# Kernel tuning notes

Hardware: AMD Instinct MI355X
Metric: run time of the kernel (lower is better)

Reference implementation:

```python
import jax, jax.numpy as jnp
import numpy as np

B, S, D, H, TOPK = 8, 128, 1024, 4096, 256


def _linear_params(key, out_d, in_d):
    # torch nn.Linear default init: U(-1/sqrt(fan_in), 1/sqrt(fan_in))
    bound = 1.0 / np.sqrt(in_d)
    kw, kb = jax.random.split(key)
    w = jax.random.uniform(kw, (out_d, in_d), minval=-bound, maxval=bound, dtype=jnp.float32)
    b = jax.random.uniform(kb, (out_d,), minval=-bound, maxval=bound, dtype=jnp.float32)
    return w, b


def setup_inputs() -> dict:
    key = jax.random.key(0)
    ks = jax.random.split(key, 6)
    inputs = jax.random.normal(ks[0], (B, S, D), dtype=jnp.float32)
    up_prev_w, up_prev_b = _linear_params(ks[1], H, D)   # self.up[0]
    up_curr_w, up_curr_b = _linear_params(ks[2], H, D)   # self.up[1]
    gate_w1, gate_b1 = _linear_params(ks[3], H, D)       # gates[0][0]
    gate_w2, gate_b2 = _linear_params(ks[4], H, H)       # gates[0][2]
    down_w, down_b = _linear_params(ks[5], D, H)         # self.down[1]
    return {
        'inputs': inputs,
        'up_prev_w': up_prev_w, 'up_prev_b': up_prev_b,
        'up_curr_w': up_curr_w, 'up_curr_b': up_curr_b,
        'gate_w1': gate_w1, 'gate_b1': gate_b1,
        'gate_w2': gate_w2, 'gate_b2': gate_b2,
        'down_w': down_w, 'down_b': down_b,
        'current_depth': 1,
    }


def reference(inputs, up_prev_w, up_prev_b, up_curr_w, up_curr_b,
              gate_w1, gate_b1, gate_w2, gate_b2, down_w, down_b,
              current_depth):
    x = inputs  # [B, S, D]
    # Gate MLP: Linear(D,H) -> ReLU -> Linear(H,H)  => scores [B, S, H]
    g = jax.nn.relu(jnp.einsum('bsd,hd->bsh', x, gate_w1) + gate_b1)
    scores = jnp.einsum('bsh,gh->bsg', g, gate_w2) + gate_b2
    # topk over flattened [S*H] scores per batch element
    k = min(TOPK * S, S * H)
    _, flat_idx = jax.lax.top_k(scores.reshape(B, S * H), k)  # [B, k]
    hidden_idx = flat_idx % H  # row indices into the weight matrices
    # Selected rows get prev layer's weights/bias (duplicate indices write the
    # same value, so a boolean-mask select is exactly equivalent to the scatter).
    sel = jnp.zeros((B, H), dtype=bool).at[jnp.arange(B)[:, None], hidden_idx].set(True)
    mod_w = jnp.where(sel[:, :, None], up_prev_w[None], up_curr_w[None])  # [B, H, D]
    mod_b = jnp.where(sel, up_prev_b[None], up_curr_b[None])              # [B, H]
    # Per-sample matmul: inputs @ mod_w^T + bias
    h = jnp.einsum('bsd,bhd->bsh', x, mod_w) + mod_b[:, None, :]
    h = jax.nn.gelu(h, approximate=False)  # torch GELU (exact)
    # dropout p=0 (eval) -> identity
    return jnp.einsum('bsh,dh->bsd', h, down_w) + down_b
```

## Files before the change

### kernel.cpp

```cpp
#include <hip/hip_runtime.h>
#include <hip/hip_bf16.h>

#define B_  8
#define S_  128
#define D_  1024
#define H_  4096
#define M_  (B_ * S_)
#define NSCORE   (M_ * H_)
#define PERBATCH (S_ * H_)
#define TOPK_K   (256 * S_)
#define BAND_CAP 8192
#define MARGIN   4e-4f

#define AS1 __attribute__((address_space(1)))
#define AS3 __attribute__((address_space(3)))

#define G_OFF    0u
#define SC_OFF   16777216u
#define GHI_OFF  33554432u
#define GLO_OFF  41943040u
#define XHI_OFF  50331648u
#define XLO_OFF  52428800u
#define W1H_OFF  54525952u
#define W1L_OFF  62914560u
#define W2H_OFF  54525952u
#define W2L_OFF  88080384u
#define WPB_OFF  54525952u
#define WCB_OFF  62914560u
#define WDB_OFF  71303168u
#define ACT_OFF  79691776u
#define H8_OFF   121634816u
#define H16_OFF  121700352u
#define SEL_OFF  123797504u
#define CNT_OFF  123928576u
#define PART_OFF 123929088u
#define BIDX_OFF 123933184u
#define BVAL_OFF 124195328u

typedef __attribute__((ext_vector_type(8))) short short8;
typedef __attribute__((ext_vector_type(4))) float f32x4;

__device__ __forceinline__ unsigned tokey(float f) {
    unsigned u = __float_as_uint(f);
    return (u & 0x80000000u) ? ~u : (u | 0x80000000u);
}
__device__ __forceinline__ float keytofloat(unsigned k) {
    unsigned u = (k & 0x80000000u) ? (k & 0x7FFFFFFFu) : ~k;
    return __uint_as_float(u);
}
__device__ __forceinline__ unsigned short bfbits(float f) {
    __hip_bfloat16 h = __float2bfloat16(f);
    return *(unsigned short*)&h;
}

__global__ __launch_bounds__(256) void split_kernel(const float* __restrict__ in,
                                                    unsigned short* __restrict__ hi,
                                                    unsigned short* __restrict__ lo, int n4) {
    int i = blockIdx.x * 256 + threadIdx.x;
    if (i >= n4) return;
    float4 v = *(const float4*)(in + (size_t)i * 4);
    unsigned short h0 = bfbits(v.x), h1 = bfbits(v.y), h2 = bfbits(v.z), h3 = bfbits(v.w);
    ushort4 hv = {h0, h1, h2, h3};
    float r0 = v.x - __bfloat162float(*(__hip_bfloat16*)&h0);
    float r1 = v.y - __bfloat162float(*(__hip_bfloat16*)&h1);
    float r2 = v.z - __bfloat162float(*(__hip_bfloat16*)&h2);
    float r3 = v.w - __bfloat162float(*(__hip_bfloat16*)&h3);
    ushort4 lv = {bfbits(r0), bfbits(r1), bfbits(r2), bfbits(r3)};
    *(ushort4*)(hi + (size_t)i*4) = hv;
    *(ushort4*)(lo + (size_t)i*4) = lv;
}

__global__ __launch_bounds__(256) void f2bf3_kernel(const float* __restrict__ s0,
                                                    const float* __restrict__ s1,
                                                    const float* __restrict__ s2,
                                                    unsigned short* __restrict__ d0,
                                                    unsigned short* __restrict__ d1,
                                                    unsigned short* __restrict__ d2) {
    const int Q = H_ * D_ / 4;
    int i = blockIdx.x * 256 + threadIdx.x;
    int w = i / Q, j = i - w * Q;
    const float* s = (w == 0) ? s0 : (w == 1) ? s1 : s2;
    unsigned short* d = (w == 0) ? d0 : (w == 1) ? d1 : d2;
    float4 v = *(const float4*)(s + (size_t)j * 4);
    ushort4 o = {bfbits(v.x), bfbits(v.y), bfbits(v.z), bfbits(v.w)};
    *(ushort4*)(d + (size_t)j * 4) = o;
}

template <int EPI>
__global__ __launch_bounds__(256) void gemm_split_kernel(const short* __restrict__ Ahg,
                                                         const short* __restrict__ Alg,
                                                         const short* __restrict__ Bhg,
                                                         const short* __restrict__ Blg,
                                                         const float* __restrict__ bias,
                                                         int K,
                                                         float* __restrict__ C,
                                                         unsigned short* __restrict__ hi,
                                                         unsigned short* __restrict__ lo) {
    __shared__ short lAh[64*64], lAl[64*64], lBh[128*64], lBl[128*64];
    const int tid = threadIdx.x, lane = tid & 63, wave = tid >> 6;
    const int row0 = blockIdx.y * 64, col0 = blockIdx.x * 128;
    f32x4 acc[4][2] = {};
    for (int kt = 0; kt < K; kt += 64) {
        #pragma unroll
        for (int q = 0; q < 2; q++) {
            int l = q * 256 + tid;
            int r = l >> 3, cg = ((l & 7) ^ (r & 7)) * 8;
            size_t go = (size_t)(row0 + r) * K + kt + cg;
            __builtin_amdgcn_global_load_lds((const AS1 unsigned*)(Ahg + go),
                (AS3 unsigned*)(lAh + l * 8), 16, 0, 0);
            __builtin_amdgcn_global_load_lds((const AS1 unsigned*)(Alg + go),
                (AS3 unsigned*)(lAl + l * 8), 16, 0, 0);
        }
        #pragma unroll
        for (int q = 0; q < 4; q++) {
            int l = q * 256 + tid;
            int r = l >> 3, cg = ((l & 7) ^ (r & 7)) * 8;
            size_t go = (size_t)(col0 + r) * K + kt + cg;
            __builtin_amdgcn_global_load_lds((const AS1 unsigned*)(Bhg + go),
                (AS3 unsigned*)(lBh + l * 8), 16, 0, 0);
            __builtin_amdgcn_global_load_lds((const AS1 unsigned*)(Blg + go),
                (AS3 unsigned*)(lBl + l * 8), 16, 0, 0);
        }
        __syncthreads();
        #pragma unroll
        for (int kk = 0; kk < 2; kk++) {
            const int cb = kk * 4 + (lane >> 4);
            short8 ah[4], al[4], bh[2], bl[2];
            #pragma unroll
            for (int i = 0; i < 4; i++) {
                int r = i * 16 + (lane & 15);
                int s = (r * 8 + (cb ^ (r & 7))) * 8;
                ah[i] = *(const short8*)(lAh + s);
                al[i] = *(const short8*)(lAl + s);
            }
            #pragma unroll
            for (int j = 0; j < 2; j++) {
                int r = wave * 32 + j * 16 + (lane & 15);
                int s = (r * 8 + (cb ^ (r & 7))) * 8;
                bh[j] = *(const short8*)(lBh + s);
                bl[j] = *(const short8*)(lBl + s);
            }
            #pragma unroll
            for (int i = 0; i < 4; i++)
                #pragma unroll
                for (int j = 0; j < 2; j++) {
                    acc[i][j] = __builtin_amdgcn_mfma_f32_16x16x32_bf16(al[i], bh[j], acc[i][j], 0, 0, 0);
                    acc[i][j] = __builtin_amdgcn_mfma_f32_16x16x32_bf16(ah[i], bl[j], acc[i][j], 0, 0, 0);
                    acc[i][j] = __builtin_amdgcn_mfma_f32_16x16x32_bf16(ah[i], bh[j], acc[i][j], 0, 0, 0);
                }
        }
        __syncthreads();
    }
    #pragma unroll
    for (int i = 0; i < 4; i++) {
        int row = row0 + i * 16 + (lane >> 4) * 4;
        #pragma unroll
        for (int j = 0; j < 2; j++) {
            int col = col0 + wave * 32 + j * 16 + (lane & 15);
            float bv = bias[col];
            #pragma unroll
            for (int r = 0; r < 4; r++) {
                float v = acc[i][j][r] + bv;
                size_t o = (size_t)(row + r) * H_ + col;
                if (EPI == 1) {
                    v = fmaxf(v, 0.0f);
                    C[o] = v;
                    unsigned short hb = bfbits(v);
                    hi[o] = hb;
                    lo[o] = bfbits(v - __bfloat162float(*(__hip_bfloat16*)&hb));
                } else {
                    C[o] = v;
                }
            }
        }
    }
}

__global__ __launch_bounds__(256) void bgemm_bt_kernel(const short* __restrict__ A,
                                                       const short* __restrict__ B0,
                                                       const short* __restrict__ B1,
                                                       float* __restrict__ C0,
                                                       float* __restrict__ C1,
                                                       int N, int K) {
    const short* Bw = (blockIdx.z == 0) ? B0 : B1;
    float*       C  = (blockIdx.z == 0) ? C0 : C1;
    __shared__ short As[128 * 32];
    __shared__ short Bs[128 * 32];
    const int tid = threadIdx.x, lane = tid & 63, wave = tid >> 6;
    const int wr = wave >> 1, wc = wave & 1;
    const int row0 = blockIdx.y * 128, col0 = blockIdx.x * 128;
    const int r_ld = tid >> 2, c_ld = (tid & 3) * 8;
    f32x4 acc[4][4] = {};
    for (int kt = 0; kt < K; kt += 32) {
        #pragma unroll
        for (int half = 0; half < 2; half++) {
            int r = half * 64 + r_ld;
            __builtin_amdgcn_global_load_lds(
                (const AS1 unsigned*)(A + (size_t)(row0 + r) * K + kt + c_ld),
                (AS3 unsigned*)(As + r * 32 + c_ld), 16, 0, 0);
            __builtin_amdgcn_global_load_lds(
                (const AS1 unsigned*)(Bw + (size_t)(col0 + r) * K + kt + c_ld),
                (AS3 unsigned*)(Bs + r * 32 + c_ld), 16, 0, 0);
        }
        __syncthreads();
        short8 af[4], bfr[4];
        #pragma unroll
        for (int t = 0; t < 4; t++) {
            af[t]  = *(const short8*)(As + (wr*64 + t*16 + (lane & 15)) * 32 + (lane >> 4) * 8);
            bfr[t] = *(const short8*)(Bs + (wc*64 + t*16 + (lane & 15)) * 32 + (lane >> 4) * 8);
        }
        #pragma unroll
        for (int tm = 0; tm < 4; tm++)
            #pragma unroll
            for (int tn = 0; tn < 4; tn++)
                acc[tm][tn] = __builtin_amdgcn_mfma_f32_16x16x32_bf16(af[tm], bfr[tn], acc[tm][tn], 0, 0, 0);
        __syncthreads();
    }
    #pragma unroll
    for (int tm = 0; tm < 4; tm++) {
        int row = row0 + wr*64 + tm*16 + (lane >> 4) * 4;
        #pragma unroll
        for (int tn = 0; tn < 4; tn++) {
            int col = col0 + wc*64 + tn*16 + (lane & 15);
            #pragma unroll
            for (int r = 0; r < 4; r++)
                C[(size_t)(row + r) * N + col] = acc[tm][tn][r];
        }
    }
}

__global__ __launch_bounds__(256) void bgemm_down_kernel(const short* __restrict__ A,
                                                         const short* __restrict__ Bw,
                                                         float* __restrict__ P) {
    __shared__ short As[128 * 32];
    __shared__ short Bs[128 * 32];
    const int tid = threadIdx.x, lane = tid & 63, wave = tid >> 6;
    const int wr = wave >> 1, wc = wave & 1;
    const int row0 = blockIdx.y * 128, col0 = blockIdx.x * 128;
    const int k0 = blockIdx.z * (H_ / 4);
    float* C = P + (size_t)blockIdx.z * (M_ * D_);
    const int r_ld = tid >> 2, c_ld = (tid & 3) * 8;
    f32x4 acc[4][4] = {};
    for (int kt = k0; kt < k0 + H_ / 4; kt += 32) {
        #pragma unroll
        for (int half = 0; half < 2; half++) {
            int r = half * 64 + r_ld;
            __builtin_amdgcn_global_load_lds(
                (const AS1 unsigned*)(A + (size_t)(row0 + r) * H_ + kt + c_ld),
                (AS3 unsigned*)(As + r * 32 + c_ld), 16, 0, 0);
            __builtin_amdgcn_global_load_lds(
                (const AS1 unsigned*)(Bw + (size_t)(col0 + r) * H_ + kt + c_ld),
                (AS3 unsigned*)(Bs + r * 32 + c_ld), 16, 0, 0);
        }
        __syncthreads();
        short8 af[4], bfr[4];
        #pragma unroll
        for (int t = 0; t < 4; t++) {
            af[t]  = *(const short8*)(As + (wr*64 + t*16 + (lane & 15)) * 32 + (lane >> 4) * 8);
            bfr[t] = *(const short8*)(Bs + (wc*64 + t*16 + (lane & 15)) * 32 + (lane >> 4) * 8);
        }
        #pragma unroll
        for (int tm = 0; tm < 4; tm++)
            #pragma unroll
            for (int tn = 0; tn < 4; tn++)
                acc[tm][tn] = __builtin_amdgcn_mfma_f32_16x16x32_bf16(af[tm], bfr[tn], acc[tm][tn], 0, 0, 0);
        __syncthreads();
    }
    #pragma unroll
    for (int tm = 0; tm < 4; tm++) {
        int row = row0 + wr*64 + tm*16 + (lane >> 4) * 4;
        #pragma unroll
        for (int tn = 0; tn < 4; tn++) {
            int col = col0 + wc*64 + tn*16 + (lane & 15);
            #pragma unroll
            for (int r = 0; r < 4; r++)
                C[(size_t)(row + r) * D_ + col] = acc[tm][tn][r];
        }
    }
}

__global__ __launch_bounds__(256) void down_merge_kernel(const float* __restrict__ P,
                                                         const float* __restrict__ db,
                                                         float* __restrict__ out) {
    int i = blockIdx.x * 256 + threadIdx.x;
    if (i >= M_ * D_ / 4) return;
    int col = (i * 4) & (D_ - 1);
    float4 a = *(const float4*)(P + (size_t)i * 4);
    float4 b = *(const float4*)(P + (size_t)(M_*D_) + (size_t)i * 4);
    float4 c = *(const float4*)(P + (size_t)(2*M_*D_) + (size_t)i * 4);
    float4 d = *(const float4*)(P + (size_t)(3*M_*D_) + (size_t)i * 4);
    float4 o;
    o.x = a.x + b.x + c.x + d.x + db[col+0];
    o.y = a.y + b.y + c.y + d.y + db[col+1];
    o.z = a.z + b.z + c.z + d.z + db[col+2];
    o.w = a.w + b.w + c.w + d.w + db[col+3];
    *(float4*)(out + (size_t)i * 4) = o;
}

__global__ __launch_bounds__(256) void hist8_kernel(const float* __restrict__ scores,
                                                    unsigned* __restrict__ h8) {
    __shared__ unsigned lh[256];
    const int b = blockIdx.y;
    lh[threadIdx.x] = 0;
    __syncthreads();
    const float* base = scores + ((size_t)b << 19) + (size_t)blockIdx.x * 8192;
    for (int j = threadIdx.x; j < 8192; j += 256) {
        unsigned key = tokey(base[j]);
        atomicAdd(&lh[key >> 24], 1u);
    }
    __syncthreads();
    unsigned v = lh[threadIdx.x];
    if (v) atomicAdd(&h8[(b << 8) + threadIdx.x], v);
}

__global__ __launch_bounds__(256) void scan8_kernel(const unsigned* __restrict__ h8,
                                                    unsigned* __restrict__ prefix1,
                                                    unsigned* __restrict__ above1) {
    int b = blockIdx.x, tid = threadIdx.x;
    __shared__ unsigned S[256];
    __shared__ int tstar;
    S[tid] = h8[(b << 8) + tid];
    __syncthreads();
    for (int off = 1; off < 256; off <<= 1) {
        unsigned a = S[tid];
        unsigned v = (tid + off < 256) ? S[tid + off] : 0u;
        __syncthreads();
        S[tid] = a + v;
        __syncthreads();
    }
    unsigned St = S[tid];
    unsigned Sn = (tid < 255) ? S[tid + 1] : 0u;
    if (St >= TOPK_K && (tid == 255 || Sn < TOPK_K)) tstar = tid;
    __syncthreads();
    if (tid == 0) {
        prefix1[b] = (unsigned)tstar;
        above1[b]  = (tstar < 255) ? S[tstar + 1] : 0u;
    }
}

__global__ __launch_bounds__(256) void hist16_kernel(const float* __restrict__ scores,
                                                     const unsigned* __restrict__ prefix1,
                                                     unsigned* __restrict__ h16) {
    int i = blockIdx.x * 256 + threadIdx.x;
    if (i >= NSCORE) return;
    int b = i >> 19;
    unsigned key = tokey(scores[i]);
    if ((key >> 24) == prefix1[b])
        atomicAdd(&h16[((size_t)b << 16) + ((key >> 8) & 0xFFFFu)], 1u);
}

__global__ __launch_bounds__(256) void scan16_kernel(const unsigned* __restrict__ h16,
                                                     const unsigned* __restrict__ prefix1,
                                                     const unsigned* __restrict__ above1,
                                                     float* __restrict__ Thi,
                                                     float* __restrict__ Tlo) {
    int b = blockIdx.x, tid = threadIdx.x;
    const unsigned* h = h16 + ((size_t)b << 16);
    unsigned k = TOPK_K - above1[b];
    __shared__ unsigned S[256];
    __shared__ int tstar;
    unsigned s = 0;
    const unsigned* seg = h + tid * 256;
    for (int i = 0; i < 256; i++) s += seg[i];
    S[tid] = s;
    __syncthreads();
    for (int off = 1; off < 256; off <<= 1) {
        unsigned a = S[tid];
        unsigned v = (tid + off < 256) ? S[tid + off] : 0u;
        __syncthreads();
        S[tid] = a + v;
        __syncthreads();
    }
    unsigned St = S[tid];
    unsigned Sn = (tid < 255) ? S[tid + 1] : 0u;
    if (St >= k && (tid == 255 || Sn < k)) tstar = tid;
    __syncthreads();
    if (tid == 0) {
        int t = tstar;
        unsigned runn = (t < 255) ? S[t + 1] : 0u;
        unsigned c = (unsigned)t * 256u;
        for (int i = 255; i >= 0; i--) {
            unsigned cc = h[t * 256 + i];
            if (runn + cc >= k) { c = (unsigned)(t * 256 + i); break; }
            runn += cc;
        }
        unsigned P24 = (prefix1[b] << 16) | c;
        float tlo = (P24 < 0x8000u) ? -INFINITY : keytofloat(P24 << 8);
        float thi = (P24 == 0x00FFFFFFu) ? INFINITY
                  : ((P24 + 1u) < 0x8000u ? -INFINITY : keytofloat((P24 + 1u) << 8));
        Thi[b] = thi + MARGIN;
        Tlo[b] = tlo - MARGIN;
    }
}

__global__ __launch_bounds__(256) void classify_kernel(const float* __restrict__ scores,
                                                       const float* __restrict__ Thi,
                                                       const float* __restrict__ Tlo,
                                                       unsigned* __restrict__ sel,
                                                       unsigned* __restrict__ partialCnt,
                                                       unsigned* __restrict__ bandN,
                                                       unsigned* __restrict__ bandIdx) {
    const int b  = blockIdx.z;
    const int h0 = blockIdx.x * 256;
    const int s0 = blockIdx.y * 16;
    const int c  = threadIdx.x;
    const float thi = Thi[b], tlo = Tlo[b];
    unsigned selbit = 0, cnt = 0;
    const float* base = scores + ((size_t)(b * S_ + s0)) * H_ + h0;
    #pragma unroll 4
    for (int j = 0; j < 16; j++) {
        float sv = base[(size_t)j * H_ + c];
        if (sv > thi) { selbit = 1u; cnt++; }
        else if (sv >= tlo) {
            unsigned slot = atomicAdd(&bandN[b], 1u);
            if (slot < BAND_CAP)
                bandIdx[(b << 13) + slot] = (unsigned)(((s0 + j) << 12) | (h0 + c));
        }
    }
    if (selbit) sel[(b << 12) + h0 + c] = 1u;
    __shared__ unsigned red[256];
    red[c] = cnt;
    __syncthreads();
    for (int off = 128; off; off >>= 1) {
        if (c < off) red[c] += red[c + off];
        __syncthreads();
    }
    if (c == 0) partialCnt[b * 128 + blockIdx.y * 16 + blockIdx.x] = red[0];
}

__global__ void finalize_cnt_kernel(const unsigned* __restrict__ partial,
                                    unsigned* __restrict__ certN) {
    int b = threadIdx.x;
    if (b >= B_) return;
    unsigned s = 0;
    for (int i = 0; i < 128; i++) s += partial[b * 128 + i];
    certN[b] = s;
}

__global__ __launch_bounds__(256) void band_exact_kernel(const float* __restrict__ g,
                                                         const float* __restrict__ w2,
                                                         const float* __restrict__ b2,
                                                         const unsigned* __restrict__ bandN,
                                                         const unsigned* __restrict__ bandIdx,
                                                         float* __restrict__ bandVal) {
    int wid = (blockIdx.x * 256 + threadIdx.x) >> 6;
    int lane = threadIdx.x & 63;
    for (int b = 0; b < B_; b++) {
        int n = bandN[b]; if (n > BAND_CAP) n = BAND_CAP;
        for (int j = wid; j < n; j += 1024) {
            unsigned f = bandIdx[(b << 13) + j];
            int m = b * S_ + (int)(f >> 12);
            int h = (int)(f & (H_ - 1));
            const float* gr = g  + (size_t)m * H_;
            const float* wr = w2 + (size_t)h * H_;
            float s = 0.0f;
            for (int cc = lane * 4; cc < H_; cc += 256) {
                float4 a = *(const float4*)(gr + cc);
                float4 w = *(const float4*)(wr + cc);
                s += a.x*w.x + a.y*w.y + a.z*w.z + a.w*w.w;
            }
            #pragma unroll
            for (int off = 32; off; off >>= 1) s += __shfl_xor(s, off);
            if (lane == 0) bandVal[(b << 13) + j] = s + b2[h];
        }
    }
}

__global__ __launch_bounds__(256) void band_select_kernel(const float* __restrict__ bandVal,
                                                          const unsigned* __restrict__ bandIdx,
                                                          const unsigned* __restrict__ bandN,
                                                          const unsigned* __restrict__ certainN,
                                                          unsigned* __restrict__ sel) {
    __shared__ float  sv[BAND_CAP];
    __shared__ unsigned si[BAND_CAP];
    int b = blockIdx.x, tid = threadIdx.x;
    int n = bandN[b]; if (n > BAND_CAP) n = BAND_CAP;
    int r = TOPK_K - (int)certainN[b];
    if (r <= 0) return;
    if (r >= n) {
        for (int j = tid; j < n; j += 256)
            sel[(b << 12) + (bandIdx[(b << 13) + j] & (H_ - 1))] = 1u;
        return;
    }
    for (int j = tid; j < n; j += 256) {
        sv[j] = bandVal[(b << 13) + j];
        si[j] = bandIdx[(b << 13) + j];
    }
    __syncthreads();
    for (int j = tid; j < n; j += 256) {
        float vj = sv[j]; unsigned fj = si[j];
        int rank = 0;
        for (int l = 0; l < n; l++) {
            float vl = sv[l]; unsigned fl = si[l];
            rank += (vl > vj) || (vl == vj && fl < fj);
        }
        if (rank < r) sel[(b << 12) + (fj & (H_ - 1))] = 1u;
    }
}

__global__ __launch_bounds__(256) void act_kernel(const float* __restrict__ hprev,
                                                  const float* __restrict__ hcurr,
                                                  const float* __restrict__ bprev,
                                                  const float* __restrict__ bcurr,
                                                  const unsigned* __restrict__ sel,
                                                  __hip_bfloat16* __restrict__ act) {
    int i = blockIdx.x * 256 + threadIdx.x;
    if (i >= NSCORE) return;
    int h = i & (H_ - 1);
    int b = i >> 19;
    float v = sel[(b << 12) + h] ? (hprev[i] + bprev[h]) : (hcurr[i] + bcurr[h]);
    float gl = 0.5f * v * (1.0f + erff(v * 0.70710678118654752440f));
    act[i] = __float2bfloat16(gl);
}

extern "C" void kernel_launch(void* const* d_in, const int* in_sizes, int n_in,
                              void* d_out, int out_size, void* d_ws, size_t ws_size,
                              hipStream_t stream) {
    const float* x     = (const float*)d_in[0];
    const float* wprev = (const float*)d_in[1];
    const float* bprev = (const float*)d_in[2];
    const float* wcurr = (const float*)d_in[3];
    const float* bcurr = (const float*)d_in[4];
    const float* gw1   = (const float*)d_in[5];
    const float* gb1   = (const float*)d_in[6];
    const float* gw2   = (const float*)d_in[7];
    const float* gb2   = (const float*)d_in[8];
    const float* dw    = (const float*)d_in[9];
    const float* db    = (const float*)d_in[10];
    float* out = (float*)d_out;
    char* ws = (char*)d_ws;

    float* g      = (float*)(ws + G_OFF);
    float* scores = (float*)(ws + SC_OFF);
    float* hprev  = (float*)(ws + G_OFF);
    float* hcurr  = (float*)(ws + SC_OFF);
    float* dpart  = (float*)(ws + GHI_OFF);
    unsigned short* ghi = (unsigned short*)(ws + GHI_OFF);
    unsigned short* glo = (unsigned short*)(ws + GLO_OFF);
    unsigned short* xhi = (unsigned short*)(ws + XHI_OFF);
    unsigned short* xlo = (unsigned short*)(ws + XLO_OFF);
    unsigned short* w1h = (unsigned short*)(ws + W1H_OFF);
    unsigned short* w1l = (unsigned short*)(ws + W1L_OFF);
    unsigned short* w2h = (unsigned short*)(ws + W2H_OFF);
    unsigned short* w2l = (unsigned short*)(ws + W2L_OFF);
    unsigned short* wpb = (unsigned short*)(ws + WPB_OFF);
    unsigned short* wcb = (unsigned short*)(ws + WCB_OFF);
    unsigned short* wdb = (unsigned short*)(ws + WDB_OFF);
    __hip_bfloat16* act = (__hip_bfloat16*)(ws + ACT_OFF);
    unsigned* h8      = (unsigned*)(ws + H8_OFF);
    unsigned* h16     = (unsigned*)(ws + H16_OFF);
    unsigned* sel     = (unsigned*)(ws + SEL_OFF);
    unsigned* certN   = (unsigned*)(ws + CNT_OFF);
    unsigned* bandN   = (unsigned*)(ws + CNT_OFF + 32);
    unsigned* prefix1 = (unsigned*)(ws + CNT_OFF + 64);
    unsigned* above1  = (unsigned*)(ws + CNT_OFF + 96);
    float*    Thi     = (float*)(ws + CNT_OFF + 128);
    float*    Tlo     = (float*)(ws + CNT_OFF + 160);
    unsigned* partCnt = (unsigned*)(ws + PART_OFF);
    unsigned* bandIdx = (unsigned*)(ws + BIDX_OFF);
    float*    bandVal = (float*)(ws + BVAL_OFF);

    hipMemsetAsync(ws + H8_OFF, 0, 65536 + 2097152, stream);
    hipMemsetAsync(ws + SEL_OFF, 0, 131072 + 512 + 4096, stream);

    split_kernel<<<(M_*D_/4 + 255)/256, 256, 0, stream>>>(x,   xhi, xlo, M_*D_/4);
    split_kernel<<<(H_*D_/4 + 255)/256, 256, 0, stream>>>(gw1, w1h, w1l, H_*D_/4);
    gemm_split_kernel<1><<<dim3(H_/128, M_/64), 256, 0, stream>>>(
        (const short*)xhi, (const short*)xlo, (const short*)w1h, (const short*)w1l,
        gb1, D_, g, ghi, glo);
    split_kernel<<<(H_*H_/4 + 255)/256, 256, 0, stream>>>(gw2, w2h, w2l, H_*H_/4);
    gemm_split_kernel<0><<<dim3(H_/128, M_/64), 256, 0, stream>>>(
        (const short*)ghi, (const short*)glo, (const short*)w2h, (const short*)w2l,
        gb2, H_, scores, nullptr, nullptr);

    f2bf3_kernel<<<3*(H_*D_/4)/256, 256, 0, stream>>>(wprev, wcurr, dw, wpb, wcb, wdb);

    hist8_kernel<<<dim3(64, 8), 256, 0, stream>>>(scores, h8);
    scan8_kernel<<<B_, 256, 0, stream>>>(h8, prefix1, above1);
    hist16_kernel<<<NSCORE/256, 256, 0, stream>>>(scores, prefix1, h16);
    scan16_kernel<<<B_, 256, 0, stream>>>(h16, prefix1, above1, Thi, Tlo);

    classify_kernel<<<dim3(16, 8, 8), 256, 0, stream>>>(scores, Thi, Tlo, sel, partCnt, bandN, bandIdx);
    finalize_cnt_kernel<<<1, 64, 0, stream>>>(partCnt, certN);
    band_exact_kernel<<<256, 256, 0, stream>>>(g, gw2, gb2, bandN, bandIdx, bandVal);
    band_select_kernel<<<B_, 256, 0, stream>>>(bandVal, bandIdx, bandN, certN, sel);

    bgemm_bt_kernel<<<dim3(H_/128, M_/128, 2), 256, 0, stream>>>(
        (const short*)xhi, (const short*)wpb, (const short*)wcb, hprev, hcurr, H_, D_);
    act_kernel<<<NSCORE/256, 256, 0, stream>>>(hprev, hcurr, bprev, bcurr, sel, act);
    bgemm_down_kernel<<<dim3(D_/128, M_/128, 4), 256, 0, stream>>>(
        (const short*)act, (const short*)wdb, dpart);
    down_merge_kernel<<<(M_*D_/4 + 255)/256, 256, 0, stream>>>(dpart, db, out);
}
```

Before: 545.2 us.

## Drop split-bf16 for gate GEMM2, fuse histogram, select-gather up GEMM with GELU

```diff
diff --git a/kernel.cpp b/kernel.cpp
--- a/kernel.cpp
+++ b/kernel.cpp
@@ -10,7 +10,7 @@
 #define PERBATCH (S_ * H_)
 #define TOPK_K   (256 * S_)
 #define BAND_CAP 8192
-#define MARGIN   4e-4f
+#define MARGIN   6e-3f
 
 #define AS1 __attribute__((address_space(1)))
 #define AS3 __attribute__((address_space(3)))
@@ -23,8 +23,7 @@
 #define XLO_OFF  52428800u
 #define W1H_OFF  54525952u
 #define W1L_OFF  62914560u
-#define W2H_OFF  54525952u
-#define W2L_OFF  88080384u
+#define W2B_OFF  54525952u
 #define WPB_OFF  54525952u
 #define WCB_OFF  62914560u
 #define WDB_OFF  71303168u
@@ -70,6 +69,15 @@
     *(ushort4*)(lo + (size_t)i*4) = lv;
 }
 
+__global__ __launch_bounds__(256) void f2bf_kernel(const float* __restrict__ in,
+                                                   unsigned short* __restrict__ out, int n4) {
+    int i = blockIdx.x * 256 + threadIdx.x;
+    if (i >= n4) return;
+    float4 v = *(const float4*)(in + (size_t)i * 4);
+    ushort4 o = {bfbits(v.x), bfbits(v.y), bfbits(v.z), bfbits(v.w)};
+    *(ushort4*)(out + (size_t)i * 4) = o;
+}
+
 __global__ __launch_bounds__(256) void f2bf3_kernel(const float* __restrict__ s0,
                                                     const float* __restrict__ s1,
                                                     const float* __restrict__ s2,
@@ -86,26 +94,23 @@
     *(ushort4*)(d + (size_t)j * 4) = o;
 }
 
-template <int EPI>
-__global__ __launch_bounds__(256) void gemm_split_kernel(const short* __restrict__ Ahg,
-                                                         const short* __restrict__ Alg,
-                                                         const short* __restrict__ Bhg,
-                                                         const short* __restrict__ Blg,
-                                                         const float* __restrict__ bias,
-                                                         int K,
-                                                         float* __restrict__ C,
-                                                         unsigned short* __restrict__ hi,
-                                                         unsigned short* __restrict__ lo) {
+__global__ __launch_bounds__(256) void gemm1_kernel(const short* __restrict__ Ahg,
+                                                    const short* __restrict__ Alg,
+                                                    const short* __restrict__ Bhg,
+                                                    const short* __restrict__ Blg,
+                                                    const float* __restrict__ bias,
+                                                    float* __restrict__ C,
+                                                    unsigned short* __restrict__ hi) {
     __shared__ short lAh[64*64], lAl[64*64], lBh[128*64], lBl[128*64];
     const int tid = threadIdx.x, lane = tid & 63, wave = tid >> 6;
     const int row0 = blockIdx.y * 64, col0 = blockIdx.x * 128;
     f32x4 acc[4][2] = {};
-    for (int kt = 0; kt < K; kt += 64) {
+    for (int kt = 0; kt < D_; kt += 64) {
         #pragma unroll
         for (int q = 0; q < 2; q++) {
             int l = q * 256 + tid;
             int r = l >> 3, cg = ((l & 7) ^ (r & 7)) * 8;
-            size_t go = (size_t)(row0 + r) * K + kt + cg;
+            size_t go = (size_t)(row0 + r) * D_ + kt + cg;
             __builtin_amdgcn_global_load_lds((const AS1 unsigned*)(Ahg + go),
                 (AS3 unsigned*)(lAh + l * 8), 16, 0, 0);
             __builtin_amdgcn_global_load_lds((const AS1 unsigned*)(Alg + go),
@@ -115,7 +120,7 @@
         for (int q = 0; q < 4; q++) {
             int l = q * 256 + tid;
             int r = l >> 3, cg = ((l & 7) ^ (r & 7)) * 8;
-            size_t go = (size_t)(col0 + r) * K + kt + cg;
+            size_t go = (size_t)(col0 + r) * D_ + kt + cg;
             __builtin_amdgcn_global_load_lds((const AS1 unsigned*)(Bhg + go),
                 (AS3 unsigned*)(lBh + l * 8), 16, 0, 0);
             __builtin_amdgcn_global_load_lds((const AS1 unsigned*)(Blg + go),
@@ -160,54 +165,123 @@
             float bv = bias[col];
             #pragma unroll
             for (int r = 0; r < 4; r++) {
+                float v = fmaxf(acc[i][j][r] + bv, 0.0f);
+                size_t o = (size_t)(row + r) * H_ + col;
+                C[o] = v;
+                hi[o] = bfbits(v);
+            }
+        }
+    }
+}
+
+__global__ __launch_bounds__(256) void gemm2_kernel(const short* __restrict__ Ahg,
+                                                    const short* __restrict__ Bhg,
+                                                    const float* __restrict__ bias,
+                                                    float* __restrict__ C,
+                                                    unsigned* __restrict__ h8) {
+    __shared__ short lAh[64*64], lBh[128*64];
+    __shared__ unsigned lh[256];
+    const int tid = threadIdx.x, lane = tid & 63, wave = tid >> 6;
+    const int row0 = blockIdx.y * 64, col0 = blockIdx.x * 128;
+    lh[tid] = 0;
+    f32x4 acc[4][2] = {};
+    for (int kt = 0; kt < H_; kt += 64) {
+        #pragma unroll
+        for (int q = 0; q < 2; q++) {
+            int l = q * 256 + tid;
+            int r = l >> 3, cg = ((l & 7) ^ (r & 7)) * 8;
+            __builtin_amdgcn_global_load_lds(
+                (const AS1 unsigned*)(Ahg + (size_t)(row0 + r) * H_ + kt + cg),
+                (AS3 unsigned*)(lAh + l * 8), 16, 0, 0);
+        }
+        #pragma unroll
+        for (int q = 0; q < 4; q++) {
+            int l = q * 256 + tid;
+            int r = l >> 3, cg = ((l & 7) ^ (r & 7)) * 8;
+            __builtin_amdgcn_global_load_lds(
+                (const AS1 unsigned*)(Bhg + (size_t)(col0 + r) * H_ + kt + cg),
+                (AS3 unsigned*)(lBh + l * 8), 16, 0, 0);
+        }
+        __syncthreads();
+        #pragma unroll
+        for (int kk = 0; kk < 2; kk++) {
+            const int cb = kk * 4 + (lane >> 4);
+            short8 ah[4], bh[2];
+            #pragma unroll
+            for (int i = 0; i < 4; i++) {
+                int r = i * 16 + (lane & 15);
+                ah[i] = *(const short8*)(lAh + (r * 8 + (cb ^ (r & 7))) * 8);
+            }
+            #pragma unroll
+            for (int j = 0; j < 2; j++) {
+                int r = wave * 32 + j * 16 + (lane & 15);
+                bh[j] = *(const short8*)(lBh + (r * 8 + (cb ^ (r & 7))) * 8);
+            }
+            #pragma unroll
+            for (int i = 0; i < 4; i++)
+                #pragma unroll
+                for (int j = 0; j < 2; j++)
+                    acc[i][j] = __builtin_amdgcn_mfma_f32_16x16x32_bf16(ah[i], bh[j], acc[i][j], 0, 0, 0);
+        }
+        __syncthreads();
+    }
+    const int b = row0 >> 7;
+    #pragma unroll
+    for (int i = 0; i < 4; i++) {
+        int row = row0 + i * 16 + (lane >> 4) * 4;
+        #pragma unroll
+        for (int j = 0; j < 2; j++) {
+            int col = col0 + wave * 32 + j * 16 + (lane & 15);
+            float bv = bias[col];
+            #pragma unroll
+            for (int r = 0; r < 4; r++) {
                 float v = acc[i][j][r] + bv;
-                size_t o = (size_t)(row + r) * H_ + col;
-                if (EPI == 1) {
-                    v = fmaxf(v, 0.0f);
-                    C[o] = v;
-                    unsigned short hb = bfbits(v);
-                    hi[o] = hb;
-                    lo[o] = bfbits(v - __bfloat162float(*(__hip_bfloat16*)&hb));
-                } else {
-                    C[o] = v;
-                }
-            }
-        }
-    }
-}
-
-__global__ __launch_bounds__(256) void bgemm_bt_kernel(const short* __restrict__ A,
-                                                       const short* __restrict__ B0,
-                                                       const short* __restrict__ B1,
-                                                       float* __restrict__ C0,
-                                                       float* __restrict__ C1,
-                                                       int N, int K) {
-    const short* Bw = (blockIdx.z == 0) ? B0 : B1;
-    float*       C  = (blockIdx.z == 0) ? C0 : C1;
+                C[(size_t)(row + r) * H_ + col] = v;
+                atomicAdd(&lh[tokey(v) >> 24], 1u);
+            }
+        }
+    }
+    __syncthreads();
+    unsigned hv = lh[tid];
+    if (hv) atomicAdd(&h8[(b << 8) + tid], hv);
+}
+
+__global__ __launch_bounds__(256) void upgemm_kernel(const short* __restrict__ A,
+                                                     const short* __restrict__ Wp,
+                                                     const short* __restrict__ Wc,
+                                                     const float* __restrict__ bp,
+                                                     const float* __restrict__ bc,
+                                                     const unsigned* __restrict__ sel,
+                                                     __hip_bfloat16* __restrict__ act) {
     __shared__ short As[128 * 32];
     __shared__ short Bs[128 * 32];
     const int tid = threadIdx.x, lane = tid & 63, wave = tid >> 6;
-    const int wr = wave >> 1, wc = wave & 1;
-    const int row0 = blockIdx.y * 128, col0 = blockIdx.x * 128;
+    const int wr = wave >> 1, wcol = wave & 1;
+    const int b = blockIdx.y;
+    const int row0 = b * 128, col0 = blockIdx.x * 128;
     const int r_ld = tid >> 2, c_ld = (tid & 3) * 8;
+    const short* B0 = sel[(b << 12) + col0 + r_ld]      ? Wp : Wc;
+    const short* B1 = sel[(b << 12) + col0 + 64 + r_ld] ? Wp : Wc;
     f32x4 acc[4][4] = {};
-    for (int kt = 0; kt < K; kt += 32) {
-        #pragma unroll
-        for (int half = 0; half < 2; half++) {
-            int r = half * 64 + r_ld;
-            __builtin_amdgcn_global_load_lds(
-                (const AS1 unsigned*)(A + (size_t)(row0 + r) * K + kt + c_ld),
-                (AS3 unsigned*)(As + r * 32 + c_ld), 16, 0, 0);
-            __builtin_amdgcn_global_load_lds(
-                (const AS1 unsigned*)(Bw + (size_t)(col0 + r) * K + kt + c_ld),
-                (AS3 unsigned*)(Bs + r * 32 + c_ld), 16, 0, 0);
-        }
+    for (int kt = 0; kt < D_; kt += 32) {
+        __builtin_amdgcn_global_load_lds(
+            (const AS1 unsigned*)(A + (size_t)(row0 + r_ld) * D_ + kt + c_ld),
+            (AS3 unsigned*)(As + r_ld * 32 + c_ld), 16, 0, 0);
+        __builtin_amdgcn_global_load_lds(
+            (const AS1 unsigned*)(A + (size_t)(row0 + 64 + r_ld) * D_ + kt + c_ld),
+            (AS3 unsigned*)(As + (64 + r_ld) * 32 + c_ld), 16, 0, 0);
+        __builtin_amdgcn_global_load_lds(
+            (const AS1 unsigned*)(B0 + (size_t)(col0 + r_ld) * D_ + kt + c_ld),
+            (AS3 unsigned*)(Bs + r_ld * 32 + c_ld), 16, 0, 0);
+        __builtin_amdgcn_global_load_lds(
+            (const AS1 unsigned*)(B1 + (size_t)(col0 + 64 + r_ld) * D_ + kt + c_ld),
+            (AS3 unsigned*)(Bs + (64 + r_ld) * 32 + c_ld), 16, 0, 0);
         __syncthreads();
         short8 af[4], bfr[4];
         #pragma unroll
         for (int t = 0; t < 4; t++) {
             af[t]  = *(const short8*)(As + (wr*64 + t*16 + (lane & 15)) * 32 + (lane >> 4) * 8);
-            bfr[t] = *(const short8*)(Bs + (wc*64 + t*16 + (lane & 15)) * 32 + (lane >> 4) * 8);
+            bfr[t] = *(const short8*)(Bs + (wcol*64 + t*16 + (lane & 15)) * 32 + (lane >> 4) * 8);
         }
         #pragma unroll
         for (int tm = 0; tm < 4; tm++)
@@ -221,10 +295,14 @@
         int row = row0 + wr*64 + tm*16 + (lane >> 4) * 4;
         #pragma unroll
         for (int tn = 0; tn < 4; tn++) {
-            int col = col0 + wc*64 + tn*16 + (lane & 15);
-            #pragma unroll
-            for (int r = 0; r < 4; r++)
-                C[(size_t)(row + r) * N + col] = acc[tm][tn][r];
+            int col = col0 + wcol*64 + tn*16 + (lane & 15);
+            float bv = sel[(b << 12) + col] ? bp[col] : bc[col];
+            #pragma unroll
+            for (int r = 0; r < 4; r++) {
+                float v = acc[tm][tn][r] + bv;
+                float gl = 0.5f * v * (1.0f + erff(v * 0.70710678118654752440f));
+                act[(size_t)(row + r) * H_ + col] = __float2bfloat16(gl);
+            }
         }
     }
 }
@@ -297,22 +375,6 @@
     *(float4*)(out + (size_t)i * 4) = o;
 }
 
-__global__ __launch_bounds__(256) void hist8_kernel(const float* __restrict__ scores,
-                                                    unsigned* __restrict__ h8) {
-    __shared__ unsigned lh[256];
-    const int b = blockIdx.y;
-    lh[threadIdx.x] = 0;
-    __syncthreads();
-    const float* base = scores + ((size_t)b << 19) + (size_t)blockIdx.x * 8192;
-    for (int j = threadIdx.x; j < 8192; j += 256) {
-        unsigned key = tokey(base[j]);
-        atomicAdd(&lh[key >> 24], 1u);
-    }
-    __syncthreads();
-    unsigned v = lh[threadIdx.x];
-    if (v) atomicAdd(&h8[(b << 8) + threadIdx.x], v);
-}
-
 __global__ __launch_bounds__(256) void scan8_kernel(const unsigned* __restrict__ h8,
                                                     unsigned* __restrict__ prefix1,
                                                     unsigned* __restrict__ above1) {
@@ -405,6 +467,11 @@
     const int s0 = blockIdx.y * 16;
     const int c  = threadIdx.x;
     const float thi = Thi[b], tlo = Tlo[b];
+    __shared__ unsigned lidx[1024];
+    __shared__ unsigned lcnt, lbase;
+    __shared__ unsigned red[256];
+    if (c == 0) lcnt = 0;
+    __syncthreads();
     unsigned selbit = 0, cnt = 0;
     const float* base = scores + ((size_t)(b * S_ + s0)) * H_ + h0;
     #pragma unroll 4
@@ -412,20 +479,27 @@
         float sv = base[(size_t)j * H_ + c];
         if (sv > thi) { selbit = 1u; cnt++; }
         else if (sv >= tlo) {
-            unsigned slot = atomicAdd(&bandN[b], 1u);
-            if (slot < BAND_CAP)
-                bandIdx[(b << 13) + slot] = (unsigned)(((s0 + j) << 12) | (h0 + c));
+            unsigned slot = atomicAdd(&lcnt, 1u);
+            if (slot < 1024u) lidx[slot] = (unsigned)(((s0 + j) << 12) | (h0 + c));
         }
     }
     if (selbit) sel[(b << 12) + h0 + c] = 1u;
-    __shared__ unsigned red[256];
     red[c] = cnt;
     __syncthreads();
     for (int off = 128; off; off >>= 1) {
         if (c < off) red[c] += red[c + off];
         __syncthreads();
     }
-    if (c == 0) partialCnt[b * 128 + blockIdx.y * 16 + blockIdx.x] = red[0];
+    unsigned nloc = lcnt > 1024u ? 1024u : lcnt;
+    if (c == 0) {
+        partialCnt[b * 128 + blockIdx.y * 16 + blockIdx.x] = red[0];
+        lbase = nloc ? atomicAdd(&bandN[b], nloc) : 0u;
+    }
+    __syncthreads();
+    for (unsigned i = c; i < nloc; i += 256) {
+        unsigned p = lbase + i;
+        if (p < BAND_CAP) bandIdx[(b << 13) + p] = lidx[i];
+    }
 }
 
 __global__ void finalize_cnt_kernel(const unsigned* __restrict__ partial,
@@ -466,51 +540,85 @@
     }
 }
 
+#define NBIN 4096
 __global__ __launch_bounds__(256) void band_select_kernel(const float* __restrict__ bandVal,
                                                           const unsigned* __restrict__ bandIdx,
                                                           const unsigned* __restrict__ bandN,
-                                                          const unsigned* __restrict__ certainN,
+                                                          const unsigned* __restrict__ certN,
+                                                          const float* __restrict__ ThiA,
+                                                          const float* __restrict__ TloA,
                                                           unsigned* __restrict__ sel) {
-    __shared__ float  sv[BAND_CAP];
-    __shared__ unsigned si[BAND_CAP];
     int b = blockIdx.x, tid = threadIdx.x;
     int n = bandN[b]; if (n > BAND_CAP) n = BAND_CAP;
-    int r = TOPK_K - (int)certainN[b];
+    int r = TOPK_K - (int)certN[b];
     if (r <= 0) return;
     if (r >= n) {
         for (int j = tid; j < n; j += 256)
             sel[(b << 12) + (bandIdx[(b << 13) + j] & (H_ - 1))] = 1u;
         return;
     }
+    const float lo = TloA[b];
+    const float scale = (float)NBIN / (ThiA[b] - lo);
+    __shared__ unsigned hist[NBIN];
+    __shared__ unsigned part[256];
+    __shared__ unsigned bstar, cabove, mcnt;
+    for (int i = tid; i < NBIN; i += 256) hist[i] = 0;
+    if (tid == 0) mcnt = 0;
+    __syncthreads();
     for (int j = tid; j < n; j += 256) {
-        sv[j] = bandVal[(b << 13) + j];
-        si[j] = bandIdx[(b << 13) + j];
-    }
-    __syncthreads();
+        float v = bandVal[(b << 13) + j];
+        int bin = (int)((v - lo) * scale);
+        bin = bin < 0 ? 0 : (bin >= NBIN ? NBIN - 1 : bin);
+        atomicAdd(&hist[bin], 1u);
+    }
+    __syncthreads();
+    unsigned s = 0;
+    for (int i = 0; i < 16; i++) s += hist[tid * 16 + i];
+    part[tid] = s;
+    __syncthreads();
+    for (int off = 1; off < 256; off <<= 1) {
+        unsigned a = part[tid];
+        unsigned v = (tid + off < 256) ? part[tid + off] : 0u;
+        __syncthreads();
+        part[tid] = a + v;
+        __syncthreads();
+    }
+    unsigned St = part[tid], Sn = (tid < 255) ? part[tid + 1] : 0u;
+    if (St >= (unsigned)r && (tid == 255 || Sn < (unsigned)r)) {
+        unsigned runn = Sn;
+        for (int i = 15; i >= 0; i--) {
+            unsigned c = hist[tid * 16 + i];
+            if (runn + c >= (unsigned)r) { bstar = (unsigned)(tid * 16 + i); cabove = runn; break; }
+            runn += c;
+        }
+    }
+    __syncthreads();
+    const int bs = (int)bstar;
+    __shared__ float  cv[512];
+    __shared__ unsigned ci[512];
     for (int j = tid; j < n; j += 256) {
-        float vj = sv[j]; unsigned fj = si[j];
+        float v = bandVal[(b << 13) + j];
+        unsigned f = bandIdx[(b << 13) + j];
+        int bin = (int)((v - lo) * scale);
+        bin = bin < 0 ? 0 : (bin >= NBIN ? NBIN - 1 : bin);
+        if (bin > bs) sel[(b << 12) + (f & (H_ - 1))] = 1u;
+        else if (bin == bs) {
+            unsigned slot = atomicAdd(&mcnt, 1u);
+            if (slot < 512u) { cv[slot] = v; ci[slot] = f; }
+        }
+    }
+    __syncthreads();
+    int need = r - (int)cabove;
+    int mm = mcnt > 512u ? 512 : (int)mcnt;
+    for (int j = tid; j < mm; j += 256) {
+        float vj = cv[j]; unsigned fj = ci[j];
         int rank = 0;
-        for (int l = 0; l < n; l++) {
-            float vl = sv[l]; unsigned fl = si[l];
+        for (int l = 0; l < mm; l++) {
+            float vl = cv[l]; unsigned fl = ci[l];
             rank += (vl > vj) || (vl == vj && fl < fj);
         }
-        if (rank < r) sel[(b << 12) + (fj & (H_ - 1))] = 1u;
-    }
-}
-
-__global__ __launch_bounds__(256) void act_kernel(const float* __restrict__ hprev,
-                                                  const float* __restrict__ hcurr,
-                                                  const float* __restrict__ bprev,
-                                                  const float* __restrict__ bcurr,
-                                                  const unsigned* __restrict__ sel,
-                                                  __hip_bfloat16* __restrict__ act) {
-    int i = blockIdx.x * 256 + threadIdx.x;
-    if (i >= NSCORE) return;
-    int h = i & (H_ - 1);
-    int b = i >> 19;
-    float v = sel[(b << 12) + h] ? (hprev[i] + bprev[h]) : (hcurr[i] + bcurr[h]);
-    float gl = 0.5f * v * (1.0f + erff(v * 0.70710678118654752440f));
-    act[i] = __float2bfloat16(gl);
+        if (rank < need) sel[(b << 12) + (fj & (H_ - 1))] = 1u;
+    }
 }
 
 extern "C" void kernel_launch(void* const* d_in, const int* in_sizes, int n_in,
@@ -532,17 +640,13 @@
 
     float* g      = (float*)(ws + G_OFF);
     float* scores = (float*)(ws + SC_OFF);
-    float* hprev  = (float*)(ws + G_OFF);
-    float* hcurr  = (float*)(ws + SC_OFF);
     float* dpart  = (float*)(ws + GHI_OFF);
     unsigned short* ghi = (unsigned short*)(ws + GHI_OFF);
-    unsigned short* glo = (unsigned short*)(ws + GLO_OFF);
     unsigned short* xhi = (unsigned short*)(ws + XHI_OFF);
     unsigned short* xlo = (unsigned short*)(ws + XLO_OFF);
     unsigned short* w1h = (unsigned short*)(ws + W1H_OFF);
     unsigned short* w1l = (unsigned short*)(ws + W1L_OFF);
-    unsigned short* w2h = (unsigned short*)(ws + W2H_OFF);
-    unsigned short* w2l = (unsigned short*)(ws + W2L_OFF);
+    unsigned short* w2b = (unsigned short*)(ws + W2B_OFF);
     unsigned short* wpb = (unsigned short*)(ws + WPB_OFF);
     unsigned short* wcb = (unsigned short*)(ws + WCB_OFF);
     unsigned short* wdb = (unsigned short*)(ws + WDB_OFF);
@@ -565,29 +669,25 @@
 
     split_kernel<<<(M_*D_/4 + 255)/256, 256, 0, stream>>>(x,   xhi, xlo, M_*D_/4);
     split_kernel<<<(H_*D_/4 + 255)/256, 256, 0, stream>>>(gw1, w1h, w1l, H_*D_/4);
-    gemm_split_kernel<1><<<dim3(H_/128, M_/64), 256, 0, stream>>>(
+    gemm1_kernel<<<dim3(H_/128, M_/64), 256, 0, stream>>>(
         (const short*)xhi, (const short*)xlo, (const short*)w1h, (const short*)w1l,
-        gb1, D_, g, ghi, glo);
-    split_kernel<<<(H_*H_/4 + 255)/256, 256, 0, stream>>>(gw2, w2h, w2l, H_*H_/4);
-    gemm_split_kernel<0><<<dim3(H_/128, M_/64), 256, 0, stream>>>(
-        (const short*)ghi, (const short*)glo, (const short*)w2h, (const short*)w2l,
-        gb2, H_, scores, nullptr, nullptr);
+        gb1, g, ghi);
+    f2bf_kernel<<<(H_*H_/4 + 255)/256, 256, 0, stream>>>(gw2, w2b, H_*H_/4);
+    gemm2_kernel<<<dim3(H_/128, M_/64), 256, 0, stream>>>(
+        (const short*)ghi, (const short*)w2b, gb2, scores, h8);
 
     f2bf3_kernel<<<3*(H_*D_/4)/256, 256, 0, stream>>>(wprev, wcurr, dw, wpb, wcb, wdb);
 
-    hist8_kernel<<<dim3(64, 8), 256, 0, stream>>>(scores, h8);
     scan8_kernel<<<B_, 256, 0, stream>>>(h8, prefix1, above1);
     hist16_kernel<<<NSCORE/256, 256, 0, stream>>>(scores, prefix1, h16);
     scan16_kernel<<<B_, 256, 0, stream>>>(h16, prefix1, above1, Thi, Tlo);
-
     classify_kernel<<<dim3(16, 8, 8), 256, 0, stream>>>(scores, Thi, Tlo, sel, partCnt, bandN, bandIdx);
     finalize_cnt_kernel<<<1, 64, 0, stream>>>(partCnt, certN);
     band_exact_kernel<<<256, 256, 0, stream>>>(g, gw2, gb2, bandN, bandIdx, bandVal);
-    band_select_kernel<<<B_, 256, 0, stream>>>(bandVal, bandIdx, bandN, certN, sel);
-
-    bgemm_bt_kernel<<<dim3(H_/128, M_/128, 2), 256, 0, stream>>>(
-        (const short*)xhi, (const short*)wpb, (const short*)wcb, hprev, hcurr, H_, D_);
-    act_kernel<<<NSCORE/256, 256, 0, stream>>>(hprev, hcurr, bprev, bcurr, sel, act);
+    band_select_kernel<<<B_, 256, 0, stream>>>(bandVal, bandIdx, bandN, certN, Thi, Tlo, sel);
+
+    upgemm_kernel<<<dim3(H_/128, B_), 256, 0, stream>>>(
+        (const short*)xhi, (const short*)wpb, (const short*)wcb, bprev, bcurr, sel, act);
     bgemm_down_kernel<<<dim3(D_/128, M_/128, 4), 256, 0, stream>>>(
         (const short*)act, (const short*)wdb, dpart);
     down_merge_kernel<<<(M_*D_/4 + 255)/256, 256, 0, stream>>>(dpart, db, out);
```

Result: slower. 614.6 us (+12.7%).
